# Performance work log

Measured on AMD Instinct MI355X. Metric: run time of the kernel, lower is better.

Reference implementation:

```python
import jax, jax.numpy as jnp
import numpy as np

V, D, H = 5000, 300, 256
B, T = 16, 512


def setup_inputs() -> dict:
    key = jax.random.key(0)
    ks = jax.random.split(key, 14)
    def w(k, shape):
        return jax.random.normal(k, shape, dtype=jnp.float32) * 0.02
    return {
        "x": jax.random.normal(ks[0], (B, T, V), dtype=jnp.float32),
        "hidden_state": jax.random.normal(ks[1], (1, H), dtype=jnp.float32),
        "context_state": jax.random.normal(ks[2], (1, H), dtype=jnp.float32),
        "E": w(ks[3], (D, V)),      # embedding Linear weight [out,in]
        "Wf": w(ks[4], (H, D)), "Uf": w(ks[5], (H, H)),
        "Wg": w(ks[6], (H, D)), "Ug": w(ks[7], (H, H)),
        "Wi": w(ks[8], (H, D)), "Ui": w(ks[9], (H, H)),
        "Wo": w(ks[10], (H, D)), "Uo": w(ks[11], (H, H)),
        "Wout": w(ks[12], (V, H)),
    }


def reference(x, hidden_state, context_state, E, Wf, Uf, Wg, Ug, Wi, Ui, Wo, Uo, Wout):
    # Precompute all input-side projections in one batched pass: [B,T,D]
    emb = jnp.einsum('btv,dv->btd', x, E)
    # Stack input-gate GEMMs: [B,T,4H]
    Wx = jnp.concatenate([Wf, Wg, Wi, Wo], axis=0)  # [4H, D]
    gates_x = jnp.einsum('btd,gd->btg', emb, Wx)    # [B, T, 4H]
    Uh = jnp.concatenate([Uf, Ug, Ui, Uo], axis=0)  # [4H, H]

    h0 = jnp.broadcast_to(hidden_state, (x.shape[0], hidden_state.shape[-1]))
    c0 = jnp.broadcast_to(context_state, (x.shape[0], context_state.shape[-1]))

    Hn = hidden_state.shape[-1]

    def step(carry, gx):
        h, c = carry
        gh = h @ Uh.T                     # [B, 4H]
        z = gx + gh
        f = jax.nn.sigmoid(z[:, 0*Hn:1*Hn])
        g = jnp.tanh(z[:, 1*Hn:2*Hn])
        i = jax.nn.sigmoid(z[:, 2*Hn:3*Hn])
        o = jax.nn.sigmoid(z[:, 3*Hn:4*Hn])
        c_new = g * i + c * f
        h_new = o * jnp.tanh(c_new)
        # NOTE: faithful to source - output projects g, not h
        out = g @ Wout.T                  # [B, V]
        return (h_new, c_new), out

    _, outs = jax.lax.scan(step, (h0, c0), jnp.swapaxes(gates_x, 0, 1))
    return jnp.swapaxes(outs, 0, 1)       # [B, T, V]
```

## Files before the change

### kernel.cpp

```cpp
#include <hip/hip_runtime.h>
#include <stdint.h>

typedef unsigned short u16;
typedef unsigned int u32;
typedef __attribute__((ext_vector_type(8))) __bf16 bf16x8;
typedef __attribute__((ext_vector_type(4))) float f32x4;
typedef __attribute__((ext_vector_type(4))) u32 u32x4;
typedef __attribute__((ext_vector_type(2))) u32 u32x2;
typedef __attribute__((ext_vector_type(4))) int i32x4;

#define DEV __device__ __forceinline__

constexpr int V = 5000, D = 300, H = 256, BB = 16, T = 512;
constexpr int M = BB * T;
constexpr int DP = 320;
constexpr int KP = 5024;
constexpr int G4 = 1024;
constexpr int NPAD = 5120;

constexpr size_t OFF_EB    = 0;
constexpr size_t OFF_WXB   = OFF_EB    + (size_t)DP * KP * 2;
constexpr size_t OFF_UHB   = OFF_WXB   + (size_t)G4 * DP * 2;
constexpr size_t OFF_WOUTB = OFF_UHB   + (size_t)G4 * H * 2;
constexpr size_t OFF_GATES = OFF_WOUTB + (size_t)NPAD * H * 2;
constexpr size_t OFF_GALL  = OFF_GATES + (size_t)T * BB * G4 * 2;

DEV u16 f2bf(float f) {
  u32 i = __builtin_bit_cast(u32, f);
  return (u16)((i + 0x7FFFu + ((i >> 16) & 1u)) >> 16);
}
DEV float bf2f(u16 u) { return __builtin_bit_cast(float, (u32)u << 16); }
DEV f32x4 MFMA(u32x4 a, u32x4 b, f32x4 c) {
  return __builtin_amdgcn_mfma_f32_16x16x32_bf16(
      __builtin_bit_cast(bf16x8, a), __builtin_bit_cast(bf16x8, b), c, 0, 0, 0);
}
DEV i32x4 MFMA8(u32x4 a, u32x4 b, i32x4 c) {
  return __builtin_amdgcn_mfma_i32_16x16x64_i8(
      __builtin_bit_cast(i32x4, a), __builtin_bit_cast(i32x4, b), c, 0, 0, 0);
}
DEV float sigm(float x) { return 1.f / (1.f + __expf(-x)); }
DEV float tanh_s(float x) { float e = __expf(2.f * x); return 1.f - 2.f / (e + 1.f); }

DEV void bar_lds() {
  asm volatile("s_waitcnt lgkmcnt(0)" ::: "memory");
  __builtin_amdgcn_sched_barrier(0);
  __builtin_amdgcn_s_barrier();
  __builtin_amdgcn_sched_barrier(0);
}

__global__ __launch_bounds__(256) void k_prep(
    const float* __restrict__ E, const float* __restrict__ Wf, const float* __restrict__ Wg,
    const float* __restrict__ Wi, const float* __restrict__ Wo,
    const float* __restrict__ Uf, const float* __restrict__ Ug,
    const float* __restrict__ Ui, const float* __restrict__ Uo,
    const float* __restrict__ Wout, char* __restrict__ ws) {
  if (blockIdx.x >= 1024) {
    char* qU = ws + OFF_UHB;
    float* zsc = (float*)(ws + OFF_UHB + (size_t)G4 * H);
    const int row = (blockIdx.x - 1024) * 4 + (threadIdx.x >> 6);
    const int lane = threadIdx.x & 63;
    const float* Up = (row < 256) ? Uf : (row < 512) ? Ug : (row < 768) ? Ui : Uo;
    f32x4 v = *(const f32x4*)(Up + (size_t)(row & 255) * H + lane * 4);
    float m = fmaxf(fmaxf(fabsf(v[0]), fabsf(v[1])), fmaxf(fabsf(v[2]), fabsf(v[3])));
    for (int i = 1; i < 64; i <<= 1) m = fmaxf(m, __shfl_xor(m, i));
    float inv = (m > 0.f) ? 127.f / m : 0.f;
    int q0 = (int)rintf(v[0] * inv), q1 = (int)rintf(v[1] * inv);
    int q2 = (int)rintf(v[2] * inv), q3 = (int)rintf(v[3] * inv);
    q0 = max(-127, min(127, q0)); q1 = max(-127, min(127, q1));
    q2 = max(-127, min(127, q2)); q3 = max(-127, min(127, q3));
    u32 pk = (u32)(q0 & 255) | ((u32)(q1 & 255) << 8) | ((u32)(q2 & 255) << 16) |
             ((u32)(q3 & 255) << 24);
    *(u32*)(qU + (size_t)row * H + lane * 4) = pk;
    if (lane == 0) zsc[row] = m / 16129.f;
    return;
  }
  u16* Eb = (u16*)(ws + OFF_EB);
  u16* Wxb = (u16*)(ws + OFF_WXB);
  u16* Wob = (u16*)(ws + OFF_WOUTB);
  const int NE = DP * KP, NW = G4 * DP, NWO = NPAD * H;
  const int total = NE + NW + NWO;
  for (int i = blockIdx.x * blockDim.x + threadIdx.x; i < total; i += 1024 * blockDim.x) {
    int j = i;
    if (j < NE) {
      int nn = j / KP, k = j % KP;
      Eb[j] = f2bf((nn < D && k < V) ? E[(size_t)nn * V + k] : 0.f);
      continue;
    }
    j -= NE;
    if (j < NW) {
      int r = j / DP, k = j % DP;
      const float* Wp = (r < 256) ? Wf : (r < 512) ? Wg : (r < 768) ? Wi : Wo;
      Wxb[j] = f2bf((k < D) ? Wp[(size_t)(r & 255) * D + k] : 0.f);
      continue;
    }
    j -= NW;
    if (j < NWO) {
      int nn = j / H, k = j % H;
      Wob[j] = f2bf((nn < V) ? Wout[(size_t)nn * H + k] : 0.f);
      continue;
    }
  }
}

__global__ __launch_bounds__(512) void k_embgates(const float* __restrict__ x,
                                                  char* __restrict__ ws) {
  __shared__ __align__(16) u16 As[32 * 40];
  __shared__ __align__(16) u16 Bs[320 * 40];
  __shared__ __align__(16) u16 embS[32 * 328];
  const u16* Eb = (const u16*)(ws + OFF_EB);
  const u16* Wxb = (const u16*)(ws + OFF_WXB);
  u16* gates = (u16*)(ws + OFF_GATES);

  const int tid = threadIdx.x;
  const int lane = tid & 63, wv = tid >> 6;
  const int l15 = lane & 15, lc = lane >> 4;
  const int it = blockIdx.x;
  const int tc = it >> 4, b = it & 15;
  const int m0x = b * T + tc * 32;

  f32x4 acc[5];
#pragma unroll
  for (int j = 0; j < 5; j++) acc[j] = (f32x4){0.f, 0.f, 0.f, 0.f};
  const int ar = tid >> 3, ak = (tid & 7) * 4;
  f32x4 xv0, xv1;
  u32x4 ev0[3], ev1[3];

#define WEMB_ISSUE(SFX, KS)                                                       \
  do {                                                                            \
    int k0_ = (KS) * 32;                                                          \
    if (tid < 256) {                                                              \
      size_t base_ = (size_t)(m0x + ar) * V + k0_ + ak;                           \
      if (k0_ + ak + 3 < V) {                                                     \
        xv##SFX = *(const f32x4*)(x + base_);                                     \
      } else {                                                                    \
        f32x4 t_;                                                                 \
        t_[0] = (k0_ + ak + 0 < V) ? x[base_ + 0] : 0.f;                          \
        t_[1] = (k0_ + ak + 1 < V) ? x[base_ + 1] : 0.f;                          \
        t_[2] = (k0_ + ak + 2 < V) ? x[base_ + 2] : 0.f;                          \
        t_[3] = (k0_ + ak + 3 < V) ? x[base_ + 3] : 0.f;                          \
        xv##SFX = t_;                                                             \
      }                                                                           \
    }                                                                             \
    _Pragma("unroll") for (int p_ = 0; p_ < 3; p_++) {                            \
      int cc_ = tid + 512 * p_;                                                   \
      if (cc_ < 1280) {                                                           \
        int n_ = cc_ >> 2, ko_ = (cc_ & 3) * 8;                                   \
        ev##SFX[p_] = *(const u32x4*)(Eb + (size_t)n_ * KP + k0_ + ko_);          \
      }                                                                           \
    }                                                                             \
  } while (0)

#define WEMB_WRITE(SFX)                                                           \
  do {                                                                            \
    if (tid < 256) {                                                              \
      union { u16 u[4]; u32x2 v; } ua_;                                           \
      ua_.u[0] = f2bf(xv##SFX[0]); ua_.u[1] = f2bf(xv##SFX[1]);                   \
      ua_.u[2] = f2bf(xv##SFX[2]); ua_.u[3] = f2bf(xv##SFX[3]);                   \
      *(u32x2*)&As[ar * 40 + ak] = ua_.v;                                         \
    }                                                                             \
    _Pragma("unroll") for (int p_ = 0; p_ < 3; p_++) {                            \
      int cc_ = tid + 512 * p_;                                                   \
      if (cc_ < 1280) {                                                           \
        int n_ = cc_ >> 2, ko_ = (cc_ & 3) * 8;                                   \
        *(u32x4*)&Bs[n_ * 40 + ko_] = ev##SFX[p_];                                \
      }                                                                           \
    }                                                                             \
  } while (0)

  const int mt = wv & 1, ntb = (wv >> 1) * 5;
  auto wemb_compute = [&]() {
    u32x4 a = *(const u32x4*)&As[(mt * 16 + l15) * 40 + lc * 8];
#pragma unroll
    for (int j = 0; j < 5; j++) {
      u32x4 bb = *(const u32x4*)&Bs[((ntb + j) * 16 + l15) * 40 + lc * 8];
      acc[j] = MFMA(a, bb, acc[j]);
    }
  };

  constexpr int NK = 157;
  WEMB_ISSUE(0, 0);
  WEMB_ISSUE(1, 1);
  for (int ks = 0; ks < NK; ks += 2) {
    __syncthreads();
    WEMB_WRITE(0);
    if (ks + 2 < NK) WEMB_ISSUE(0, ks + 2);
    __syncthreads();
    wemb_compute();
    if (ks + 1 < NK) {
      __syncthreads();
      WEMB_WRITE(1);
      if (ks + 3 < NK) WEMB_ISSUE(1, ks + 3);
      __syncthreads();
      wemb_compute();
    }
  }
#undef WEMB_ISSUE
#undef WEMB_WRITE
  __syncthreads();
#pragma unroll
  for (int j = 0; j < 5; j++) {
    int nn = (ntb + j) * 16 + l15;
#pragma unroll
    for (int r = 0; r < 4; r++)
      embS[(mt * 16 + lc * 4 + r) * 328 + nn] = f2bf(acc[j][r]);
  }
  __syncthreads();

  const int amt = wv & 1, ngrp = wv >> 1;
  f32x4 gacc[16];
#pragma unroll
  for (int j = 0; j < 16; j++) gacc[j] = (f32x4){0.f, 0.f, 0.f, 0.f};
#pragma unroll 1
  for (int kc = 0; kc < 10; kc++) {
    u32x4 a = *(const u32x4*)&embS[(amt * 16 + l15) * 328 + kc * 32 + lc * 8];
#pragma unroll
    for (int nt = 0; nt < 16; nt++) {
      int col = ngrp * 256 + nt * 16 + l15;
      u32x4 bb = *(const u32x4*)(Wxb + (size_t)col * DP + kc * 32 + lc * 8);
      gacc[nt] = MFMA(a, bb, gacc[nt]);
    }
  }
#pragma unroll
  for (int nt = 0; nt < 16; nt++) {
#pragma unroll
    for (int r = 0; r < 4; r++) {
      int t = tc * 32 + amt * 16 + lc * 4 + r;
      int col = ngrp * 256 + nt * 16 + l15;
      int q = col >> 8, nn = col & 255;
      gates[(((size_t)t * 16 + b) * 256 + nn) * 4 + q] = f2bf(gacc[nt][r]);
    }
  }
}

__global__ __launch_bounds__(512) void k_scan(const float* __restrict__ hidden,
                                              const float* __restrict__ ctx,
                                              char* __restrict__ ws) {
  const char* qU = (const char*)(ws + OFF_UHB);
  const float* zsc = (const float*)(ws + OFF_UHB + (size_t)G4 * H);
  const u16* gates = (const u16*)(ws + OFF_GATES);
  u16* gall = (u16*)(ws + OFF_GALL);

  __shared__ __align__(16) char pq[2][2][256];
  __shared__ __align__(16) int zw[2][8][8][2][16];

  const int tid = threadIdx.x;
  const int lane = tid & 63, wv = tid >> 6;
  const int l15 = lane & 15, lc = lane >> 4;

  u32x4 uq[4][2][4];
#pragma unroll
  for (int gg = 0; gg < 4; gg++)
#pragma unroll
    for (int j = 0; j < 2; j++)
#pragma unroll
      for (int kt = 0; kt < 4; kt++)
        uq[gg][j][kt] = *(const u32x4*)(
            qU + (size_t)(gg * 256 + wv * 32 + j * 16 + l15) * H + kt * 64 + lc * 16);

  const int b = lane >> 5, np = lane & 31;
  const int n = wv * 32 + np;
  const int jj = (np >> 4) & 1, rr = np & 15;
  const int b_glob = blockIdx.x * 2 + b;
  float c = ctx[n];
  const float zs0 = zsc[n], zs1 = zsc[n + 256], zs2 = zsc[n + 512], zs3 = zsc[n + 768];
  u32x2 gxc = *(const u32x2*)(gates + (((size_t)0 * 16 + b_glob) * 256 + n) * 4);
  u32x2 gxn = *(const u32x2*)(gates + (((size_t)1 * 16 + b_glob) * 256 + n) * 4);

  {
    const int b0 = tid >> 8, n0i = tid & 255;
    float h0 = hidden[n0i];
    h0 = fminf(3.999f, fmaxf(-3.999f, h0));
    pq[0][b0][n0i] = (char)(int)rintf(h0 * 31.75f);
  }
  __syncthreads();

#pragma unroll 1
  for (int t = 0; t < T; ++t) {
    const int par = t & 1;
    u32x4 bfr[4];
#pragma unroll
    for (int kt = 0; kt < 4; kt++)
      bfr[kt] = *(const u32x4*)&pq[par][l15 & 1][kt * 64 + lc * 16];

    i32x4 acc[4][2];
#pragma unroll
    for (int gg = 0; gg < 4; gg++)
#pragma unroll
      for (int j = 0; j < 2; j++) {
        i32x4 a = {0, 0, 0, 0};
#pragma unroll
        for (int kt = 0; kt < 4; kt++) a = MFMA8(uq[gg][j][kt], bfr[kt], a);
        acc[gg][j] = a;
      }
    if (l15 < 2) {
#pragma unroll
      for (int gg = 0; gg < 4; gg++)
#pragma unroll
        for (int j = 0; j < 2; j++)
          *(i32x4*)&zw[par][wv][gg * 2 + j][l15][lc * 4] = acc[gg][j];
    }
    asm volatile("s_waitcnt lgkmcnt(0)" ::: "memory");
    __builtin_amdgcn_sched_barrier(0);

    const float hs = (t == 0) ? 4.f : 1.f;
    float z0 = (float)zw[par][wv][0 + jj][b][rr] * (zs0 * hs) + bf2f((u16)(gxc[0] & 0xFFFFu));
    float z1 = (float)zw[par][wv][2 + jj][b][rr] * (zs1 * hs) + bf2f((u16)(gxc[0] >> 16));
    float z2 = (float)zw[par][wv][4 + jj][b][rr] * (zs2 * hs) + bf2f((u16)(gxc[1] & 0xFFFFu));
    float z3 = (float)zw[par][wv][6 + jj][b][rr] * (zs3 * hs) + bf2f((u16)(gxc[1] >> 16));
    float fv = sigm(z0), gv = tanh_s(z1), iv = sigm(z2), ov = sigm(z3);
    c = gv * iv + c * fv;
    float hn = ov * tanh_s(c);
    gall[((size_t)b_glob * T + t) * H + n] = f2bf(gv);
    pq[par ^ 1][b][n] = (char)(int)rintf(hn * 127.f);
    gxc = gxn;
    int t2 = (t + 2 < T) ? (t + 2) : t;
    gxn = *(const u32x2*)(gates + (((size_t)t2 * 16 + b_glob) * 256 + n) * 4);
    bar_lds();
  }
}

__global__ __launch_bounds__(256) void k_out(char* __restrict__ ws, float* __restrict__ out) {
  const u16* gall = (const u16*)(ws + OFF_GALL);
  const u16* Wob = (const u16*)(ws + OFF_WOUTB);
  __shared__ __align__(16) u16 As[64 * 40];
  __shared__ __align__(16) u16 Bs[256 * 40];
  __shared__ __align__(16) float tb[64 * 132];

  const int tid = threadIdx.x;
  const int blk = blockIdx.x;
  const int m0 = (blk / 20) * 64, n0 = (blk % 20) * 256;
  const int lane = tid & 63, wv = tid >> 6;
  const int l15 = lane & 15, lc = lane >> 4;

  f32x4 acc[16];
#pragma unroll
  for (int j = 0; j < 16; j++) acc[j] = (f32x4){0.f, 0.f, 0.f, 0.f};

  u32x4 av0, av1;
  u32x4 bv0[4], bv1[4];

#define OUT_ISSUE(SFX, KS)                                                        \
  do {                                                                            \
    int k0_ = (KS) * 32;                                                          \
    {                                                                             \
      int r_ = tid >> 2, ko_ = (tid & 3) * 8;                                     \
      av##SFX = *(const u32x4*)(gall + (size_t)(m0 + r_) * H + k0_ + ko_);        \
    }                                                                             \
    _Pragma("unroll") for (int j_ = 0; j_ < 4; j_++) {                            \
      int c_ = tid + 256 * j_;                                                    \
      int n_ = c_ >> 2, ko_ = (c_ & 3) * 8;                                       \
      bv##SFX[j_] = *(const u32x4*)(Wob + (size_t)(n0 + n_) * H + k0_ + ko_);     \
    }                                                                             \
  } while (0)

#define OUT_WRITE(SFX)                                                            \
  do {                                                                            \
    {                                                                             \
      int r_ = tid >> 2, ko_ = (tid & 3) * 8;                                     \
      *(u32x4*)&As[r_ * 40 + ko_] = av##SFX;                                      \
    }                                                                             \
    _Pragma("unroll") for (int j_ = 0; j_ < 4; j_++) {                            \
      int c_ = tid + 256 * j_;                                                    \
      int n_ = c_ >> 2, ko_ = (c_ & 3) * 8;                                       \
      *(u32x4*)&Bs[n_ * 40 + ko_] = bv##SFX[j_];                                  \
    }                                                                             \
  } while (0)

  auto out_compute = [&]() {
    u32x4 a = *(const u32x4*)&As[(wv * 16 + l15) * 40 + lc * 8];
#pragma unroll
    for (int nt = 0; nt < 16; nt++) {
      u32x4 b = *(const u32x4*)&Bs[(nt * 16 + l15) * 40 + lc * 8];
      acc[nt] = MFMA(a, b, acc[nt]);
    }
  };

  constexpr int NK = 8;
  OUT_ISSUE(0, 0);
  OUT_ISSUE(1, 1);
  for (int ks = 0; ks < NK; ks += 2) {
    __syncthreads();
    OUT_WRITE(0);
    if (ks + 2 < NK) OUT_ISSUE(0, ks + 2);
    __syncthreads();
    out_compute();
    __syncthreads();
    OUT_WRITE(1);
    if (ks + 3 < NK) OUT_ISSUE(1, ks + 3);
    __syncthreads();
    out_compute();
  }

#pragma unroll
  for (int h = 0; h < 2; h++) {
    __syncthreads();
#pragma unroll
    for (int nt = 0; nt < 8; nt++) {
#pragma unroll
      for (int r = 0; r < 4; r++)
        tb[(wv * 16 + lc * 4 + r) * 132 + nt * 16 + l15] = acc[h * 8 + nt][r];
    }
    __syncthreads();
#pragma unroll
    for (int cc = 0; cc < 8; cc++) {
      int idx = cc * 256 + tid;
      int row = idx >> 5, c4 = (idx & 31) * 4;
      int gcol = n0 + h * 128 + c4;
      if (gcol + 3 < V) {
        f32x4 v = *(const f32x4*)&tb[row * 132 + c4];
        *(f32x4*)&out[(size_t)(m0 + row) * V + gcol] = v;
      }
    }
  }
#undef OUT_ISSUE
#undef OUT_WRITE
}

extern "C" void kernel_launch(void* const* d_in, const int* in_sizes, int n_in,
                              void* d_out, int out_size, void* d_ws, size_t ws_size,
                              hipStream_t stream) {
  (void)in_sizes; (void)n_in; (void)out_size; (void)ws_size;
  const float* x      = (const float*)d_in[0];
  const float* hidden = (const float*)d_in[1];
  const float* ctx    = (const float*)d_in[2];
  const float* E      = (const float*)d_in[3];
  const float* Wf     = (const float*)d_in[4];
  const float* Uf     = (const float*)d_in[5];
  const float* Wg     = (const float*)d_in[6];
  const float* Ug     = (const float*)d_in[7];
  const float* Wi     = (const float*)d_in[8];
  const float* Ui     = (const float*)d_in[9];
  const float* Wo     = (const float*)d_in[10];
  const float* Uo     = (const float*)d_in[11];
  const float* Wout   = (const float*)d_in[12];
  char* ws = (char*)d_ws;
  float* out = (float*)d_out;

  hipLaunchKernelGGL(k_prep, dim3(1280), dim3(256), 0, stream,
                     E, Wf, Wg, Wi, Wo, Uf, Ug, Ui, Uo, Wout, ws);
  hipLaunchKernelGGL(k_embgates, dim3(256), dim3(512), 0, stream, x, ws);
  hipLaunchKernelGGL(k_scan, dim3(8), dim3(512), 0, stream, hidden, ctx, ws);
  hipLaunchKernelGGL(k_out, dim3((M / 64) * 20), dim3(256), 0, stream, ws, out);
}
```

Before: 822.6 us.

## Double embedding tile rows per block and unroll scan loop by two

Measured after the change: 858.1 us. 4.3% more time.

```diff
diff --git a/kernel.cpp b/kernel.cpp
--- a/kernel.cpp
+++ b/kernel.cpp
@@ -104,9 +104,10 @@
 
 __global__ __launch_bounds__(512) void k_embgates(const float* __restrict__ x,
                                                   char* __restrict__ ws) {
-  __shared__ __align__(16) u16 As[32 * 40];
-  __shared__ __align__(16) u16 Bs[320 * 40];
-  __shared__ __align__(16) u16 embS[32 * 328];
+  __shared__ __align__(16) char sm[42112];
+  u16* As = (u16*)sm;
+  u16* Bs = (u16*)(sm + 5120);
+  u16* embS = (u16*)sm;
   const u16* Eb = (const u16*)(ws + OFF_EB);
   const u16* Wxb = (const u16*)(ws + OFF_WXB);
   u16* gates = (u16*)(ws + OFF_GATES);
@@ -116,11 +117,11 @@
   const int l15 = lane & 15, lc = lane >> 4;
   const int it = blockIdx.x;
   const int tc = it >> 4, b = it & 15;
-  const int m0x = b * T + tc * 32;
-
-  f32x4 acc[5];
-#pragma unroll
-  for (int j = 0; j < 5; j++) acc[j] = (f32x4){0.f, 0.f, 0.f, 0.f};
+  const int m0x = b * T + tc * 64;
+
+  f32x4 acc[10];
+#pragma unroll
+  for (int j = 0; j < 10; j++) acc[j] = (f32x4){0.f, 0.f, 0.f, 0.f};
   const int ar = tid >> 3, ak = (tid & 7) * 4;
   f32x4 xv0, xv1;
   u32x4 ev0[3], ev1[3];
@@ -128,7 +129,7 @@
 #define WEMB_ISSUE(SFX, KS)                                                       \
   do {                                                                            \
     int k0_ = (KS) * 32;                                                          \
-    if (tid < 256) {                                                              \
+    {                                                                             \
       size_t base_ = (size_t)(m0x + ar) * V + k0_ + ak;                           \
       if (k0_ + ak + 3 < V) {                                                     \
         xv##SFX = *(const f32x4*)(x + base_);                                     \
@@ -152,7 +153,7 @@
 
 #define WEMB_WRITE(SFX)                                                           \
   do {                                                                            \
-    if (tid < 256) {                                                              \
+    {                                                                             \
       union { u16 u[4]; u32x2 v; } ua_;                                           \
       ua_.u[0] = f2bf(xv##SFX[0]); ua_.u[1] = f2bf(xv##SFX[1]);                   \
       ua_.u[2] = f2bf(xv##SFX[2]); ua_.u[3] = f2bf(xv##SFX[3]);                   \
@@ -167,12 +168,12 @@
     }                                                                             \
   } while (0)
 
-  const int mt = wv & 1, ntb = (wv >> 1) * 5;
+  const int mt = wv >> 1, nh = wv & 1;
   auto wemb_compute = [&]() {
     u32x4 a = *(const u32x4*)&As[(mt * 16 + l15) * 40 + lc * 8];
 #pragma unroll
-    for (int j = 0; j < 5; j++) {
-      u32x4 bb = *(const u32x4*)&Bs[((ntb + j) * 16 + l15) * 40 + lc * 8];
+    for (int j = 0; j < 10; j++) {
+      u32x4 bb = *(const u32x4*)&Bs[((nh * 10 + j) * 16 + l15) * 40 + lc * 8];
       acc[j] = MFMA(a, bb, acc[j]);
     }
   };
@@ -198,8 +199,8 @@
 #undef WEMB_WRITE
   __syncthreads();
 #pragma unroll
-  for (int j = 0; j < 5; j++) {
-    int nn = (ntb + j) * 16 + l15;
+  for (int j = 0; j < 10; j++) {
+    int nn = (nh * 10 + j) * 16 + l15;
 #pragma unroll
     for (int r = 0; r < 4; r++)
       embS[(mt * 16 + lc * 4 + r) * 328 + nn] = f2bf(acc[j][r]);
@@ -207,27 +208,30 @@
   __syncthreads();
 
   const int amt = wv & 1, ngrp = wv >> 1;
-  f32x4 gacc[16];
-#pragma unroll
-  for (int j = 0; j < 16; j++) gacc[j] = (f32x4){0.f, 0.f, 0.f, 0.f};
 #pragma unroll 1
-  for (int kc = 0; kc < 10; kc++) {
-    u32x4 a = *(const u32x4*)&embS[(amt * 16 + l15) * 328 + kc * 32 + lc * 8];
+  for (int p = 0; p < 2; p++) {
+    f32x4 gacc[16];
+#pragma unroll
+    for (int j = 0; j < 16; j++) gacc[j] = (f32x4){0.f, 0.f, 0.f, 0.f};
+#pragma unroll 1
+    for (int kc = 0; kc < 10; kc++) {
+      u32x4 a = *(const u32x4*)&embS[(p * 32 + amt * 16 + l15) * 328 + kc * 32 + lc * 8];
+#pragma unroll
+      for (int nt = 0; nt < 16; nt++) {
+        int col = ngrp * 256 + nt * 16 + l15;
+        u32x4 bb = *(const u32x4*)(Wxb + (size_t)col * DP + kc * 32 + lc * 8);
+        gacc[nt] = MFMA(a, bb, gacc[nt]);
+      }
+    }
 #pragma unroll
     for (int nt = 0; nt < 16; nt++) {
-      int col = ngrp * 256 + nt * 16 + l15;
-      u32x4 bb = *(const u32x4*)(Wxb + (size_t)col * DP + kc * 32 + lc * 8);
-      gacc[nt] = MFMA(a, bb, gacc[nt]);
-    }
-  }
-#pragma unroll
-  for (int nt = 0; nt < 16; nt++) {
-#pragma unroll
-    for (int r = 0; r < 4; r++) {
-      int t = tc * 32 + amt * 16 + lc * 4 + r;
-      int col = ngrp * 256 + nt * 16 + l15;
-      int q = col >> 8, nn = col & 255;
-      gates[(((size_t)t * 16 + b) * 256 + nn) * 4 + q] = f2bf(gacc[nt][r]);
+#pragma unroll
+      for (int r = 0; r < 4; r++) {
+        int t = tc * 64 + p * 32 + amt * 16 + lc * 4 + r;
+        int col = ngrp * 256 + nt * 16 + l15;
+        int q = col >> 8, nn = col & 255;
+        gates[(((size_t)t * 16 + b) * 256 + nn) * 4 + q] = f2bf(gacc[nt][r]);
+      }
     }
   }
 }
@@ -265,6 +269,8 @@
   const float zs0 = zsc[n], zs1 = zsc[n + 256], zs2 = zsc[n + 512], zs3 = zsc[n + 768];
   u32x2 gxc = *(const u32x2*)(gates + (((size_t)0 * 16 + b_glob) * 256 + n) * 4);
   u32x2 gxn = *(const u32x2*)(gates + (((size_t)1 * 16 + b_glob) * 256 + n) * 4);
+  const u16* gxp = gates + (((size_t)2 * 16 + b_glob) * 256 + n) * 4;
+  u16* gallp = gall + (size_t)b_glob * T * H + n;
 
   {
     const int b0 = tid >> 8, n0i = tid & 255;
@@ -274,49 +280,50 @@
   }
   __syncthreads();
 
+#define SCAN_STEP(PAR, S0, S1, S2, S3)                                                     \
+  {                                                                                        \
+    u32x4 bfr[4];                                                                          \
+    _Pragma("unroll") for (int kt = 0; kt < 4; kt++)                                       \
+        bfr[kt] = *(const u32x4*)&pq[PAR][l15 & 1][kt * 64 + lc * 16];                     \
+    i32x4 acc[4][2];                                                                       \
+    _Pragma("unroll") for (int gg = 0; gg < 4; gg++)                                       \
+        _Pragma("unroll") for (int j = 0; j < 2; j++) {                                    \
+      i32x4 a = {0, 0, 0, 0};                                                              \
+      _Pragma("unroll") for (int kt = 0; kt < 4; kt++)                                     \
+          a = MFMA8(uq[gg][j][kt], bfr[kt], a);                                            \
+      acc[gg][j] = a;                                                                      \
+    }                                                                                      \
+    if (l15 < 2) {                                                                         \
+      _Pragma("unroll") for (int gg = 0; gg < 4; gg++)                                     \
+          _Pragma("unroll") for (int j = 0; j < 2; j++)                                    \
+              *(i32x4*)&zw[PAR][wv][gg * 2 + j][l15][lc * 4] = acc[gg][j];                 \
+    }                                                                                      \
+    asm volatile("s_waitcnt lgkmcnt(0)" ::: "memory");                                     \
+    __builtin_amdgcn_sched_barrier(0);                                                     \
+    float z0 = (float)zw[PAR][wv][0 + jj][b][rr] * (S0) + bf2f((u16)(gxc[0] & 0xFFFFu));   \
+    float z1 = (float)zw[PAR][wv][2 + jj][b][rr] * (S1) + bf2f((u16)(gxc[0] >> 16));       \
+    float z2 = (float)zw[PAR][wv][4 + jj][b][rr] * (S2) + bf2f((u16)(gxc[1] & 0xFFFFu));   \
+    float z3 = (float)zw[PAR][wv][6 + jj][b][rr] * (S3) + bf2f((u16)(gxc[1] >> 16));       \
+    float fv = sigm(z0), gv = tanh_s(z1), iv = sigm(z2), ov = sigm(z3);                    \
+    c = gv * iv + c * fv;                                                                  \
+    float hn = ov * tanh_s(c);                                                             \
+    *gallp = f2bf(gv);                                                                     \
+    gallp += H;                                                                            \
+    pq[(PAR) ^ 1][b][n] = (char)(int)rintf(hn * 127.f);                                    \
+    gxc = gxn;                                                                             \
+    gxn = *(const u32x2*)gxp;                                                              \
+    gxp += 16384;                                                  \
+    bar_lds();                                                                             \
+  }
+
+  SCAN_STEP(0, zs0 * 4.f, zs1 * 4.f, zs2 * 4.f, zs3 * 4.f)
 #pragma unroll 1
-  for (int t = 0; t < T; ++t) {
-    const int par = t & 1;
-    u32x4 bfr[4];
-#pragma unroll
-    for (int kt = 0; kt < 4; kt++)
-      bfr[kt] = *(const u32x4*)&pq[par][l15 & 1][kt * 64 + lc * 16];
-
-    i32x4 acc[4][2];
-#pragma unroll
-    for (int gg = 0; gg < 4; gg++)
-#pragma unroll
-      for (int j = 0; j < 2; j++) {
-        i32x4 a = {0, 0, 0, 0};
-#pragma unroll
-        for (int kt = 0; kt < 4; kt++) a = MFMA8(uq[gg][j][kt], bfr[kt], a);
-        acc[gg][j] = a;
-      }
-    if (l15 < 2) {
-#pragma unroll
-      for (int gg = 0; gg < 4; gg++)
-#pragma unroll
-        for (int j = 0; j < 2; j++)
-          *(i32x4*)&zw[par][wv][gg * 2 + j][l15][lc * 4] = acc[gg][j];
-    }
-    asm volatile("s_waitcnt lgkmcnt(0)" ::: "memory");
-    __builtin_amdgcn_sched_barrier(0);
-
-    const float hs = (t == 0) ? 4.f : 1.f;
-    float z0 = (float)zw[par][wv][0 + jj][b][rr] * (zs0 * hs) + bf2f((u16)(gxc[0] & 0xFFFFu));
-    float z1 = (float)zw[par][wv][2 + jj][b][rr] * (zs1 * hs) + bf2f((u16)(gxc[0] >> 16));
-    float z2 = (float)zw[par][wv][4 + jj][b][rr] * (zs2 * hs) + bf2f((u16)(gxc[1] & 0xFFFFu));
-    float z3 = (float)zw[par][wv][6 + jj][b][rr] * (zs3 * hs) + bf2f((u16)(gxc[1] >> 16));
-    float fv = sigm(z0), gv = tanh_s(z1), iv = sigm(z2), ov = sigm(z3);
-    c = gv * iv + c * fv;
-    float hn = ov * tanh_s(c);
-    gall[((size_t)b_glob * T + t) * H + n] = f2bf(gv);
-    pq[par ^ 1][b][n] = (char)(int)rintf(hn * 127.f);
-    gxc = gxn;
-    int t2 = (t + 2 < T) ? (t + 2) : t;
-    gxn = *(const u32x2*)(gates + (((size_t)t2 * 16 + b_glob) * 256 + n) * 4);
-    bar_lds();
-  }
+  for (int t = 1; t + 1 < T; t += 2) {
+    SCAN_STEP(1, zs0, zs1, zs2, zs3)
+    SCAN_STEP(0, zs0, zs1, zs2, zs3)
+  }
+  SCAN_STEP(1, zs0, zs1, zs2, zs3)
+#undef SCAN_STEP
 }
 
 __global__ __launch_bounds__(256) void k_out(char* __restrict__ ws, float* __restrict__ out) {
@@ -438,7 +445,7 @@
 
   hipLaunchKernelGGL(k_prep, dim3(1280), dim3(256), 0, stream,
                      E, Wf, Wg, Wi, Wo, Uf, Ug, Ui, Uo, Wout, ws);
-  hipLaunchKernelGGL(k_embgates, dim3(256), dim3(512), 0, stream, x, ws);
+  hipLaunchKernelGGL(k_embgates, dim3(128), dim3(512), 0, stream, x, ws);
   hipLaunchKernelGGL(k_scan, dim3(8), dim3(512), 0, stream, hidden, ctx, ws);
   hipLaunchKernelGGL(k_out, dim3((M / 64) * 20), dim3(256), 0, stream, ws, out);
 }
```
